# Optimization experiments

Hardware: AMD Instinct MI355X
Metric: run time of the kernel (lower is better)

The kernel has to match this reference:

```python
import jax, jax.numpy as jnp
import numpy as np

EMBED_DIM = 512
N_HEADS = 8
HEAD_DIM = EMBED_DIM // N_HEADS
B, S = 4, 2048

def gelu(x):
    # torch F.gelu default = exact erf gelu
    return jax.nn.gelu(x, approximate=False)

def setup_inputs() -> dict:
    key = jax.random.key(0)
    ks = jax.random.split(key, 9)
    sc = 1.0 / np.sqrt(EMBED_DIM)
    inp = {
        'x':   jax.random.normal(ks[0], (B, S, EMBED_DIM), dtype=jnp.float32),
        'Wq':  jax.random.uniform(ks[1], (EMBED_DIM, EMBED_DIM), jnp.float32, -sc, sc),
        'bq':  jax.random.uniform(ks[2], (EMBED_DIM,), jnp.float32, -sc, sc),
        'Wk':  jax.random.uniform(ks[3], (EMBED_DIM, EMBED_DIM), jnp.float32, -sc, sc),
        'bk':  jax.random.uniform(ks[4], (EMBED_DIM,), jnp.float32, -sc, sc),
        'Wv':  jax.random.uniform(ks[5], (EMBED_DIM, EMBED_DIM), jnp.float32, -sc, sc),
        'bv':  jax.random.uniform(ks[6], (EMBED_DIM,), jnp.float32, -sc, sc),
        'Wo':  jax.random.uniform(ks[7], (EMBED_DIM, EMBED_DIM), jnp.float32, -sc, sc),
        'bo':  jax.random.uniform(ks[8], (EMBED_DIM,), jnp.float32, -sc, sc),
    }
    return inp

def reference(x, Wq, bq, Wk, bk, Wv, bv, Wo, bo):
    Bsz, Ssz, _ = x.shape
    def proj(W, b):
        # [B,S,E] -> [B,H,S,D], GELU applied before head split (same math either way)
        h = gelu(jnp.einsum('bse,ef->bsf', x, W.T) + b)
        return h.reshape(Bsz, Ssz, N_HEADS, HEAD_DIM).transpose(0, 2, 1, 3)
    q = proj(Wq, bq)
    k = proj(Wk, bk)
    v = proj(Wv, bv)
    attn = jnp.einsum('bhid,bhjd->bhij', q, k) / np.sqrt(HEAD_DIM).astype(np.float32)
    attn = jax.nn.softmax(attn, axis=-1)
    o = jnp.einsum('bhij,bhjd->bhid', attn, v)
    o = o.transpose(0, 2, 1, 3).reshape(Bsz, Ssz, EMBED_DIM)
    return gelu(jnp.einsum('bse,ef->bsf', o, Wo.T) + bo)
```

## Files before the change

### kernel.cpp

```cpp
#include <hip/hip_runtime.h>
#include <hip/hip_bf16.h>

typedef __bf16 bf16_t;
typedef __bf16 bf16x4 __attribute__((ext_vector_type(4)));
typedef __bf16 bf16x8 __attribute__((ext_vector_type(8)));
typedef float  f32x4  __attribute__((ext_vector_type(4)));
typedef float  f32x8  __attribute__((ext_vector_type(8)));

#define EMBED 512
#define NH    8
#define HD    64
#define SEQ   2048
#define MTOT  8192
#define SCQ   0.18033688011112042f

__device__ __forceinline__ float gelu_f(float x) {
    return 0.5f * x * (1.0f + erff(x * 0.7071067811865475f));
}

__device__ __forceinline__ f32x4 mfma16(bf16x8 a, bf16x8 b, f32x4 c) {
    return __builtin_amdgcn_mfma_f32_16x16x32_bf16(a, b, c, 0, 0, 0);
}

__global__ __launch_bounds__(256)
void convert_kernel(const float* __restrict__ x,  const float* __restrict__ Wq,
                    const float* __restrict__ Wk, const float* __restrict__ Wv,
                    bf16_t* __restrict__ xb, bf16_t* __restrict__ wb)
{
    const int y = blockIdx.y;
    const float* src; bf16_t* dst;
    if (y < 16)      { src = x + (size_t)y * 262144; dst = xb + (size_t)y * 262144; }
    else if (y == 16){ src = Wq; dst = wb; }
    else if (y == 17){ src = Wk; dst = wb + 262144; }
    else             { src = Wv; dst = wb + 524288; }
    const int base = (blockIdx.x * 256 + threadIdx.x) * 16;
    const f32x8 a = *(const f32x8*)(src + base);
    const f32x8 b = *(const f32x8*)(src + base + 8);
    *(bf16x8*)(dst + base)     = __builtin_convertvector(a, bf16x8);
    *(bf16x8*)(dst + base + 8) = __builtin_convertvector(b, bf16x8);
}

template<int MODE, int NTILE>
__global__ __launch_bounds__(256, 3)
void gemm_gelu_kernel(const bf16_t* __restrict__ Xb,
                      const bf16_t* __restrict__ Wb,
                      const float*  __restrict__ Wf,
                      const float*  __restrict__ B0,
                      const float*  __restrict__ B1,
                      bf16_t* __restrict__ O0, bf16_t* __restrict__ O1,
                      bf16_t* __restrict__ O2, float* __restrict__ Of)
{
    constexpr int NTN = NTILE / 32;
    __shared__ __align__(16) bf16_t SMEM[128 * 72 + NTILE * 72];
    bf16_t* As = SMEM;
    bf16_t* Bs = SMEM + 128 * 72;
    const int tid  = threadIdx.x;
    const int lane = tid & 63, w = tid >> 6, quad = lane >> 4, l15 = lane & 15;
    const int m0 = blockIdx.x * 128;
    int mat, n0;
    if (MODE == 0) { mat = blockIdx.y >> 2; n0 = (blockIdx.y & 3) * 128; }
    else           { mat = 2;               n0 = blockIdx.y * NTILE; }
    const bf16_t* W  = (MODE == 2) ? nullptr
                                   : (Wb + (size_t)((MODE == 0) ? mat : 2) * 262144);
    const float*  Bi = (MODE == 0) ? (mat == 0 ? B0 : B1) : B0;

    const int wr = (w >> 1) * 64;
    const int wc = (w & 1) * (NTILE / 2);
    const int srow = tid >> 3, scol = (tid & 7) * 8;

    f32x4 acc[4][NTN];
#pragma unroll
    for (int a = 0; a < 4; ++a)
#pragma unroll
        for (int b = 0; b < NTN; ++b) acc[a][b] = f32x4{0.f, 0.f, 0.f, 0.f};

    bf16x8 xp[4];
    bf16x8 wpb[NTN];
    f32x8  wpf[NTN];

#pragma unroll
    for (int it = 0; it < 4; ++it)
        xp[it] = *(const bf16x8*)(Xb + (size_t)(m0 + it * 32 + srow) * EMBED + scol);
#pragma unroll
    for (int it = 0; it < NTN; ++it) {
        const int r = it * 32 + srow;
        if (MODE != 2) wpb[it] = *(const bf16x8*)(W + (size_t)(n0 + r) * EMBED + scol);
        else           wpf[it] = *(const f32x8*)(Wf + (size_t)(n0 + r) * EMBED + scol);
    }

#pragma unroll 1
    for (int kt = 0; kt < 8; ++kt) {
        __syncthreads();
#pragma unroll
        for (int it = 0; it < 4; ++it)
            *(bf16x8*)(As + (it * 32 + srow) * 72 + scol) = xp[it];
#pragma unroll
        for (int it = 0; it < NTN; ++it) {
            const int r = it * 32 + srow;
            if (MODE != 2) *(bf16x8*)(Bs + r * 72 + scol) = wpb[it];
            else *(bf16x8*)(Bs + r * 72 + scol) = __builtin_convertvector(wpf[it], bf16x8);
        }
        if (kt < 7) {
            const int k1 = (kt + 1) * 64;
#pragma unroll
            for (int it = 0; it < 4; ++it)
                xp[it] = *(const bf16x8*)(Xb + (size_t)(m0 + it * 32 + srow) * EMBED + k1 + scol);
#pragma unroll
            for (int it = 0; it < NTN; ++it) {
                const int r = it * 32 + srow;
                if (MODE != 2) wpb[it] = *(const bf16x8*)(W + (size_t)(n0 + r) * EMBED + k1 + scol);
                else           wpf[it] = *(const f32x8*)(Wf + (size_t)(n0 + r) * EMBED + k1 + scol);
            }
        }
        __syncthreads();
#pragma unroll
        for (int ks = 0; ks < 2; ++ks) {
            const int ko = (ks * 4 + quad) * 8;
            bf16x8 av[4], bv[NTN];
#pragma unroll
            for (int mt = 0; mt < 4; ++mt)
                av[mt] = *(const bf16x8*)(As + (wr + mt * 16 + l15) * 72 + ko);
#pragma unroll
            for (int nt = 0; nt < NTN; ++nt)
                bv[nt] = *(const bf16x8*)(Bs + (wc + nt * 16 + l15) * 72 + ko);
            if (MODE == 0) {
#pragma unroll
                for (int a = 0; a < NTN; ++a)
#pragma unroll
                    for (int b = 0; b < 4; ++b)
                        acc[a][b] = mfma16(bv[a], av[b], acc[a][b]);
            } else {
#pragma unroll
                for (int a = 0; a < 4; ++a)
#pragma unroll
                    for (int b = 0; b < NTN; ++b)
                        acc[a][b] = mfma16(av[a], bv[b], acc[a][b]);
            }
        }
    }

    if (MODE == 0) {
        bf16_t* T = SMEM;
        __syncthreads();
        const float scl = (mat == 0) ? SCQ : 1.0f;
#pragma unroll
        for (int at = 0; at < 4; ++at) {
            const int nb = wc + at * 16 + quad * 4;
            const f32x4 b4 = *(const f32x4*)(Bi + n0 + nb);
#pragma unroll
            for (int bt = 0; bt < 4; ++bt) {
                const int m = wr + bt * 16 + l15;
                bf16x4 pk;
#pragma unroll
                for (int i = 0; i < 4; ++i)
                    pk[i] = (bf16_t)(gelu_f(acc[at][bt][i] + b4[i]) * scl);
                *(bf16x4*)(T + m * 136 + nb) = pk;
            }
        }
        __syncthreads();
        bf16_t* O = (mat == 0) ? O0 : O1;
#pragma unroll
        for (int it = 0; it < 8; ++it) {
            const int chunk = w * 8 + it;
            const int hh = chunk >> 4, sg = chunk & 15;
            const int sr = lane >> 3, dc = (lane & 7) * 8;
            const int m = m0 + sg * 8 + sr;
            const int bb = m >> 11, s = m & (SEQ - 1);
            const int h = (n0 + hh * 64) >> 6;
            const bf16x8 v = *(const bf16x8*)(T + (sg * 8 + sr) * 136 + hh * 64 + dc);
            *(bf16x8*)(O + (((size_t)(bb * NH + h)) * SEQ + s) * HD + dc) = v;
        }
    } else if (MODE == 1) {
        bf16_t* T = SMEM;
        __syncthreads();
#pragma unroll
        for (int mt = 0; mt < 4; ++mt) {
            const int mloc = wr + mt * 16 + quad * 4;
#pragma unroll
            for (int nt = 0; nt < 4; ++nt) {
                const int nloc = wc + nt * 16 + l15;
                const float bs = Bi[n0 + nloc];
                bf16x4 pk;
#pragma unroll
                for (int i = 0; i < 4; ++i)
                    pk[i] = (bf16_t)gelu_f(acc[mt][nt][i] + bs);
                *(bf16x4*)(T + nloc * 136 + mloc) = pk;
            }
        }
        __syncthreads();
        const int bb = m0 >> 11, sbase = m0 & (SEQ - 1);
#pragma unroll
        for (int it = 0; it < 8; ++it) {
            const int chunk = w * 8 + it;
            const int r = lane >> 4, sc = (lane & 15) * 8;
            const int nloc = chunk * 4 + r;
            const int fc = n0 + nloc, h = fc >> 6, d = fc & 63;
            const bf16x8 v = *(const bf16x8*)(T + nloc * 136 + sc);
            *(bf16x8*)(O2 + ((size_t)(bb * NH + h) * HD + d) * SEQ + sbase + sc) = v;
        }
    } else {
#pragma unroll
        for (int mt = 0; mt < 4; ++mt) {
            const int mb = m0 + wr + mt * 16 + quad * 4;
#pragma unroll
            for (int nt = 0; nt < NTN; ++nt) {
                const int fc = n0 + wc + nt * 16 + l15;
                const float bs = Bi[fc];
#pragma unroll
                for (int i = 0; i < 4; ++i)
                    Of[(size_t)(mb + i) * EMBED + fc] = gelu_f(acc[mt][nt][i] + bs);
            }
        }
    }
}

__global__ __launch_bounds__(256, 2)
void flash_attn_kernel(const bf16_t* __restrict__ Q,
                       const bf16_t* __restrict__ K,
                       const bf16_t* __restrict__ Vt,
                       bf16_t* __restrict__ Og)
{
    __shared__ __align__(16) bf16_t Ks[2][64 * 72];
    __shared__ __align__(16) bf16_t Vs[2][64 * 72];
    __shared__ __align__(16) bf16_t Ps[4][32 * 72];

    const int tid  = threadIdx.x;
    const int lane = tid & 63, w = tid >> 6, quad = lane >> 4, l15 = lane & 15;
    const int bh = blockIdx.y;
    const int q0 = blockIdx.x * 128;
    const size_t baseQK = (size_t)bh * SEQ * HD;
    const size_t baseV  = (size_t)bh * HD * SEQ;
    const int wm = w * 32;

    bf16x8 qf[2][2];
#pragma unroll
    for (int mt = 0; mt < 2; ++mt)
#pragma unroll
        for (int ks = 0; ks < 2; ++ks)
            qf[mt][ks] = *(const bf16x8*)(Q + baseQK +
                (size_t)(q0 + wm + mt * 16 + l15) * HD + ks * 32 + quad * 8);

    float lsum[2] = {0.f, 0.f};
    f32x4 oacc[2][4];
#pragma unroll
    for (int mt = 0; mt < 2; ++mt)
#pragma unroll
        for (int nt = 0; nt < 4; ++nt) oacc[mt][nt] = f32x4{0.f, 0.f, 0.f, 0.f};

    bf16_t* Pw = Ps[w];
    const int r0 = tid >> 3, c0 = (tid & 7) * 8;
    bf16x8 kr0, kr1, vr0, vr1;

    kr0 = *(const bf16x8*)(K + baseQK + (size_t)r0 * HD + c0);
    kr1 = *(const bf16x8*)(K + baseQK + (size_t)(r0 + 32) * HD + c0);
    vr0 = *(const bf16x8*)(Vt + baseV + (size_t)r0 * SEQ + c0);
    vr1 = *(const bf16x8*)(Vt + baseV + (size_t)(r0 + 32) * SEQ + c0);
    *(bf16x8*)(Ks[0] + r0 * 72 + c0)        = kr0;
    *(bf16x8*)(Ks[0] + (r0 + 32) * 72 + c0) = kr1;
    *(bf16x8*)(Vs[0] + r0 * 72 + c0)        = vr0;
    *(bf16x8*)(Vs[0] + (r0 + 32) * 72 + c0) = vr1;
    kr0 = *(const bf16x8*)(K + baseQK + (size_t)(64 + r0) * HD + c0);
    kr1 = *(const bf16x8*)(K + baseQK + (size_t)(64 + r0 + 32) * HD + c0);
    vr0 = *(const bf16x8*)(Vt + baseV + (size_t)r0 * SEQ + 64 + c0);
    vr1 = *(const bf16x8*)(Vt + baseV + (size_t)(r0 + 32) * SEQ + 64 + c0);

#pragma unroll 1
    for (int t = 0; t < 32; ++t) {
        __syncthreads();
        if (t + 1 < 32) {
            bf16_t* Kn = Ks[(t + 1) & 1];
            bf16_t* Vn = Vs[(t + 1) & 1];
            *(bf16x8*)(Kn + r0 * 72 + c0)        = kr0;
            *(bf16x8*)(Kn + (r0 + 32) * 72 + c0) = kr1;
            *(bf16x8*)(Vn + r0 * 72 + c0)        = vr0;
            *(bf16x8*)(Vn + (r0 + 32) * 72 + c0) = vr1;
        }
        if (t + 2 < 32) {
            const int kv = (t + 2) * 64;
            kr0 = *(const bf16x8*)(K + baseQK + (size_t)(kv + r0) * HD + c0);
            kr1 = *(const bf16x8*)(K + baseQK + (size_t)(kv + r0 + 32) * HD + c0);
            vr0 = *(const bf16x8*)(Vt + baseV + (size_t)r0 * SEQ + kv + c0);
            vr1 = *(const bf16x8*)(Vt + baseV + (size_t)(r0 + 32) * SEQ + kv + c0);
        }

        const bf16_t* Kb = Ks[t & 1];
        const bf16_t* Vb = Vs[t & 1];

        f32x4 sf[2][4];
#pragma unroll
        for (int mt = 0; mt < 2; ++mt)
#pragma unroll
            for (int jt = 0; jt < 4; ++jt) sf[mt][jt] = f32x4{0.f, 0.f, 0.f, 0.f};
#pragma unroll
        for (int ks = 0; ks < 2; ++ks) {
            const int ko = ks * 32 + quad * 8;
#pragma unroll
            for (int jt = 0; jt < 4; ++jt) {
                const bf16x8 a = *(const bf16x8*)(Kb + (jt * 16 + l15) * 72 + ko);
                sf[0][jt] = mfma16(a, qf[0][ks], sf[0][jt]);
                sf[1][jt] = mfma16(a, qf[1][ks], sf[1][jt]);
            }
        }

#pragma unroll
        for (int mt = 0; mt < 2; ++mt)
#pragma unroll
            for (int jt = 0; jt < 4; ++jt) {
                f32x4 p;
#pragma unroll
                for (int i = 0; i < 4; ++i) {
                    p[i] = exp2f(sf[mt][jt][i] - 8.f);
                    lsum[mt] += p[i];
                }
                const bf16x4 pk = __builtin_convertvector(p, bf16x4);
                *(bf16x4*)(Pw + (mt * 16 + l15) * 72 + jt * 16 + quad * 4) = pk;
            }

#pragma unroll
        for (int c = 0; c < 2; ++c) {
            const int ko = c * 32 + quad * 8;
            const bf16x8 a0 = *(const bf16x8*)(Pw + l15 * 72 + ko);
            const bf16x8 a1 = *(const bf16x8*)(Pw + (16 + l15) * 72 + ko);
#pragma unroll
            for (int nt = 0; nt < 4; ++nt) {
                const bf16x8 b = *(const bf16x8*)(Vb + (nt * 16 + l15) * 72 + ko);
                oacc[0][nt] = mfma16(a0, b, oacc[0][nt]);
                oacc[1][nt] = mfma16(a1, b, oacc[1][nt]);
            }
        }
    }

    const int bidx = bh >> 3, h = bh & 7;
#pragma unroll
    for (int mt = 0; mt < 2; ++mt) {
        float rs = lsum[mt];
        rs += __shfl_xor(rs, 16);
        rs += __shfl_xor(rs, 32);
        float lf[4];
#pragma unroll
        for (int i = 0; i < 4; ++i)
            lf[i] = __shfl(rs, (lane & 48) | (quad * 4 + i));
#pragma unroll
        for (int nt = 0; nt < 4; ++nt)
#pragma unroll
            for (int i = 0; i < 4; ++i) {
                const int s = q0 + wm + mt * 16 + quad * 4 + i;
                const int d = nt * 16 + l15;
                Og[((size_t)(bidx * SEQ + s)) * EMBED + h * HD + d] =
                    (bf16_t)(oacc[mt][nt][i] / lf[i]);
            }
    }
}

extern "C" void kernel_launch(void* const* d_in, const int* in_sizes, int n_in,
                              void* d_out, int out_size, void* d_ws, size_t ws_size,
                              hipStream_t stream)
{
    const float* x  = (const float*)d_in[0];
    const float* Wq = (const float*)d_in[1];
    const float* bq = (const float*)d_in[2];
    const float* Wk = (const float*)d_in[3];
    const float* bk = (const float*)d_in[4];
    const float* Wv = (const float*)d_in[5];
    const float* bv = (const float*)d_in[6];
    const float* Wo = (const float*)d_in[7];
    const float* bo = (const float*)d_in[8];
    float* out = (float*)d_out;

    const size_t NE = (size_t)MTOT * EMBED;
    bf16_t* xb  = (bf16_t*)d_out;
    bf16_t* Qw  = (bf16_t*)d_out + NE;
    bf16_t* Kw  = (bf16_t*)d_ws;
    bf16_t* Vtw = Kw + NE;
    bf16_t* Ow  = Vtw + NE;
    bf16_t* Wb  = Ow;

    convert_kernel<<<dim3(64, 19), 256, 0, stream>>>(x, Wq, Wk, Wv, xb, Wb);
    gemm_gelu_kernel<0, 128><<<dim3(64, 8), 256, 0, stream>>>(
        xb, Wb, nullptr, bq, bk, Qw, Kw, nullptr, nullptr);
    gemm_gelu_kernel<1, 128><<<dim3(64, 4), 256, 0, stream>>>(
        xb, Wb, nullptr, bv, nullptr, nullptr, nullptr, Vtw, nullptr);
    flash_attn_kernel<<<dim3(16, 32), 256, 0, stream>>>(Qw, Kw, Vtw, Ow);
    gemm_gelu_kernel<2, 64><<<dim3(64, 8), 256, 0, stream>>>(
        Ow, nullptr, Wo, bo, nullptr, nullptr, nullptr, nullptr, out);
}
```

Measured before the change: 199.3 us.

## Fuse V projection into QK GEMM launch and unpad flash-attn K/V LDS

```diff
diff --git a/kernel.cpp b/kernel.cpp
--- a/kernel.cpp
+++ b/kernel.cpp
@@ -47,6 +47,7 @@
                       const float*  __restrict__ Wf,
                       const float*  __restrict__ B0,
                       const float*  __restrict__ B1,
+                      const float*  __restrict__ B2,
                       bf16_t* __restrict__ O0, bf16_t* __restrict__ O1,
                       bf16_t* __restrict__ O2, float* __restrict__ Of)
 {
@@ -59,10 +60,9 @@
     const int m0 = blockIdx.x * 128;
     int mat, n0;
     if (MODE == 0) { mat = blockIdx.y >> 2; n0 = (blockIdx.y & 3) * 128; }
-    else           { mat = 2;               n0 = blockIdx.y * NTILE; }
-    const bf16_t* W  = (MODE == 2) ? nullptr
-                                   : (Wb + (size_t)((MODE == 0) ? mat : 2) * 262144);
-    const float*  Bi = (MODE == 0) ? (mat == 0 ? B0 : B1) : B0;
+    else           { mat = 0;               n0 = blockIdx.y * NTILE; }
+    const bf16_t* W  = (MODE == 0) ? (Wb + (size_t)mat * 262144) : nullptr;
+    const float*  Bi = (MODE == 0) ? (mat == 0 ? B0 : (mat == 1 ? B1 : B2)) : B0;
 
     const int wr = (w >> 1) * 64;
     const int wc = (w & 1) * (NTILE / 2);
@@ -84,7 +84,7 @@
 #pragma unroll
     for (int it = 0; it < NTN; ++it) {
         const int r = it * 32 + srow;
-        if (MODE != 2) wpb[it] = *(const bf16x8*)(W + (size_t)(n0 + r) * EMBED + scol);
+        if (MODE == 0) wpb[it] = *(const bf16x8*)(W + (size_t)(n0 + r) * EMBED + scol);
         else           wpf[it] = *(const f32x8*)(Wf + (size_t)(n0 + r) * EMBED + scol);
     }
 
@@ -97,7 +97,7 @@
 #pragma unroll
         for (int it = 0; it < NTN; ++it) {
             const int r = it * 32 + srow;
-            if (MODE != 2) *(bf16x8*)(Bs + r * 72 + scol) = wpb[it];
+            if (MODE == 0) *(bf16x8*)(Bs + r * 72 + scol) = wpb[it];
             else *(bf16x8*)(Bs + r * 72 + scol) = __builtin_convertvector(wpf[it], bf16x8);
         }
         if (kt < 7) {
@@ -108,7 +108,7 @@
 #pragma unroll
             for (int it = 0; it < NTN; ++it) {
                 const int r = it * 32 + srow;
-                if (MODE != 2) wpb[it] = *(const bf16x8*)(W + (size_t)(n0 + r) * EMBED + k1 + scol);
+                if (MODE == 0) wpb[it] = *(const bf16x8*)(W + (size_t)(n0 + r) * EMBED + k1 + scol);
                 else           wpf[it] = *(const f32x8*)(Wf + (size_t)(n0 + r) * EMBED + k1 + scol);
             }
         }
@@ -142,61 +142,61 @@
     if (MODE == 0) {
         bf16_t* T = SMEM;
         __syncthreads();
-        const float scl = (mat == 0) ? SCQ : 1.0f;
-#pragma unroll
-        for (int at = 0; at < 4; ++at) {
-            const int nb = wc + at * 16 + quad * 4;
-            const f32x4 b4 = *(const f32x4*)(Bi + n0 + nb);
-#pragma unroll
-            for (int bt = 0; bt < 4; ++bt) {
-                const int m = wr + bt * 16 + l15;
-                bf16x4 pk;
-#pragma unroll
-                for (int i = 0; i < 4; ++i)
-                    pk[i] = (bf16_t)(gelu_f(acc[at][bt][i] + b4[i]) * scl);
-                *(bf16x4*)(T + m * 136 + nb) = pk;
-            }
-        }
-        __syncthreads();
-        bf16_t* O = (mat == 0) ? O0 : O1;
-#pragma unroll
-        for (int it = 0; it < 8; ++it) {
-            const int chunk = w * 8 + it;
-            const int hh = chunk >> 4, sg = chunk & 15;
-            const int sr = lane >> 3, dc = (lane & 7) * 8;
-            const int m = m0 + sg * 8 + sr;
-            const int bb = m >> 11, s = m & (SEQ - 1);
-            const int h = (n0 + hh * 64) >> 6;
-            const bf16x8 v = *(const bf16x8*)(T + (sg * 8 + sr) * 136 + hh * 64 + dc);
-            *(bf16x8*)(O + (((size_t)(bb * NH + h)) * SEQ + s) * HD + dc) = v;
-        }
-    } else if (MODE == 1) {
-        bf16_t* T = SMEM;
-        __syncthreads();
-#pragma unroll
-        for (int mt = 0; mt < 4; ++mt) {
-            const int mloc = wr + mt * 16 + quad * 4;
-#pragma unroll
-            for (int nt = 0; nt < 4; ++nt) {
-                const int nloc = wc + nt * 16 + l15;
-                const float bs = Bi[n0 + nloc];
-                bf16x4 pk;
-#pragma unroll
-                for (int i = 0; i < 4; ++i)
-                    pk[i] = (bf16_t)gelu_f(acc[mt][nt][i] + bs);
-                *(bf16x4*)(T + nloc * 136 + mloc) = pk;
-            }
-        }
-        __syncthreads();
-        const int bb = m0 >> 11, sbase = m0 & (SEQ - 1);
-#pragma unroll
-        for (int it = 0; it < 8; ++it) {
-            const int chunk = w * 8 + it;
-            const int r = lane >> 4, sc = (lane & 15) * 8;
-            const int nloc = chunk * 4 + r;
-            const int fc = n0 + nloc, h = fc >> 6, d = fc & 63;
-            const bf16x8 v = *(const bf16x8*)(T + nloc * 136 + sc);
-            *(bf16x8*)(O2 + ((size_t)(bb * NH + h) * HD + d) * SEQ + sbase + sc) = v;
+        if (mat < 2) {
+            const float scl = (mat == 0) ? SCQ : 1.0f;
+#pragma unroll
+            for (int at = 0; at < 4; ++at) {
+                const int nb = wc + at * 16 + quad * 4;
+                const f32x4 b4 = *(const f32x4*)(Bi + n0 + nb);
+#pragma unroll
+                for (int bt = 0; bt < 4; ++bt) {
+                    const int m = wr + bt * 16 + l15;
+                    bf16x4 pk;
+#pragma unroll
+                    for (int i = 0; i < 4; ++i)
+                        pk[i] = (bf16_t)(gelu_f(acc[at][bt][i] + b4[i]) * scl);
+                    *(bf16x4*)(T + m * 136 + nb) = pk;
+                }
+            }
+        } else {
+#pragma unroll
+            for (int at = 0; at < 4; ++at) {
+                const int nb = wc + at * 16 + quad * 4;
+                const f32x4 b4 = *(const f32x4*)(Bi + n0 + nb);
+#pragma unroll
+                for (int bt = 0; bt < 4; ++bt) {
+                    const int m = wr + bt * 16 + l15;
+#pragma unroll
+                    for (int i = 0; i < 4; ++i)
+                        T[(nb + i) * 136 + m] = (bf16_t)gelu_f(acc[at][bt][i] + b4[i]);
+                }
+            }
+        }
+        __syncthreads();
+        if (mat < 2) {
+            bf16_t* O = (mat == 0) ? O0 : O1;
+#pragma unroll
+            for (int it = 0; it < 8; ++it) {
+                const int chunk = w * 8 + it;
+                const int hh = chunk >> 4, sg = chunk & 15;
+                const int sr = lane >> 3, dc = (lane & 7) * 8;
+                const int m = m0 + sg * 8 + sr;
+                const int bb = m >> 11, s = m & (SEQ - 1);
+                const int h = (n0 + hh * 64) >> 6;
+                const bf16x8 v = *(const bf16x8*)(T + (sg * 8 + sr) * 136 + hh * 64 + dc);
+                *(bf16x8*)(O + (((size_t)(bb * NH + h)) * SEQ + s) * HD + dc) = v;
+            }
+        } else {
+            const int bb = m0 >> 11, sbase = m0 & (SEQ - 1);
+#pragma unroll
+            for (int it = 0; it < 8; ++it) {
+                const int chunk = w * 8 + it;
+                const int r = lane >> 4, sc = (lane & 15) * 8;
+                const int nloc = chunk * 4 + r;
+                const int fc = n0 + nloc, h = fc >> 6, d = fc & 63;
+                const bf16x8 v = *(const bf16x8*)(T + nloc * 136 + sc);
+                *(bf16x8*)(O2 + ((size_t)(bb * NH + h) * HD + d) * SEQ + sbase + sc) = v;
+            }
         }
     } else {
 #pragma unroll
@@ -214,14 +214,14 @@
     }
 }
 
-__global__ __launch_bounds__(256, 2)
+__global__ __launch_bounds__(256, 3)
 void flash_attn_kernel(const bf16_t* __restrict__ Q,
                        const bf16_t* __restrict__ K,
                        const bf16_t* __restrict__ Vt,
                        bf16_t* __restrict__ Og)
 {
-    __shared__ __align__(16) bf16_t Ks[2][64 * 72];
-    __shared__ __align__(16) bf16_t Vs[2][64 * 72];
+    __shared__ __align__(16) bf16_t Ks[2][64 * 64];
+    __shared__ __align__(16) bf16_t Vs[2][64 * 64];
     __shared__ __align__(16) bf16_t Ps[4][32 * 72];
 
     const int tid  = threadIdx.x;
@@ -255,10 +255,10 @@
     kr1 = *(const bf16x8*)(K + baseQK + (size_t)(r0 + 32) * HD + c0);
     vr0 = *(const bf16x8*)(Vt + baseV + (size_t)r0 * SEQ + c0);
     vr1 = *(const bf16x8*)(Vt + baseV + (size_t)(r0 + 32) * SEQ + c0);
-    *(bf16x8*)(Ks[0] + r0 * 72 + c0)        = kr0;
-    *(bf16x8*)(Ks[0] + (r0 + 32) * 72 + c0) = kr1;
-    *(bf16x8*)(Vs[0] + r0 * 72 + c0)        = vr0;
-    *(bf16x8*)(Vs[0] + (r0 + 32) * 72 + c0) = vr1;
+    *(bf16x8*)(Ks[0] + r0 * 64 + c0)        = kr0;
+    *(bf16x8*)(Ks[0] + (r0 + 32) * 64 + c0) = kr1;
+    *(bf16x8*)(Vs[0] + r0 * 64 + c0)        = vr0;
+    *(bf16x8*)(Vs[0] + (r0 + 32) * 64 + c0) = vr1;
     kr0 = *(const bf16x8*)(K + baseQK + (size_t)(64 + r0) * HD + c0);
     kr1 = *(const bf16x8*)(K + baseQK + (size_t)(64 + r0 + 32) * HD + c0);
     vr0 = *(const bf16x8*)(Vt + baseV + (size_t)r0 * SEQ + 64 + c0);
@@ -270,10 +270,10 @@
         if (t + 1 < 32) {
             bf16_t* Kn = Ks[(t + 1) & 1];
             bf16_t* Vn = Vs[(t + 1) & 1];
-            *(bf16x8*)(Kn + r0 * 72 + c0)        = kr0;
-            *(bf16x8*)(Kn + (r0 + 32) * 72 + c0) = kr1;
-            *(bf16x8*)(Vn + r0 * 72 + c0)        = vr0;
-            *(bf16x8*)(Vn + (r0 + 32) * 72 + c0) = vr1;
+            *(bf16x8*)(Kn + r0 * 64 + c0)        = kr0;
+            *(bf16x8*)(Kn + (r0 + 32) * 64 + c0) = kr1;
+            *(bf16x8*)(Vn + r0 * 64 + c0)        = vr0;
+            *(bf16x8*)(Vn + (r0 + 32) * 64 + c0) = vr1;
         }
         if (t + 2 < 32) {
             const int kv = (t + 2) * 64;
@@ -296,7 +296,7 @@
             const int ko = ks * 32 + quad * 8;
 #pragma unroll
             for (int jt = 0; jt < 4; ++jt) {
-                const bf16x8 a = *(const bf16x8*)(Kb + (jt * 16 + l15) * 72 + ko);
+                const bf16x8 a = *(const bf16x8*)(Kb + (jt * 16 + l15) * 64 + ko);
                 sf[0][jt] = mfma16(a, qf[0][ks], sf[0][jt]);
                 sf[1][jt] = mfma16(a, qf[1][ks], sf[1][jt]);
             }
@@ -323,7 +323,7 @@
             const bf16x8 a1 = *(const bf16x8*)(Pw + (16 + l15) * 72 + ko);
 #pragma unroll
             for (int nt = 0; nt < 4; ++nt) {
-                const bf16x8 b = *(const bf16x8*)(Vb + (nt * 16 + l15) * 72 + ko);
+                const bf16x8 b = *(const bf16x8*)(Vb + (nt * 16 + l15) * 64 + ko);
                 oacc[0][nt] = mfma16(a0, b, oacc[0][nt]);
                 oacc[1][nt] = mfma16(a1, b, oacc[1][nt]);
             }
@@ -376,11 +376,9 @@
     bf16_t* Wb  = Ow;
 
     convert_kernel<<<dim3(64, 19), 256, 0, stream>>>(x, Wq, Wk, Wv, xb, Wb);
-    gemm_gelu_kernel<0, 128><<<dim3(64, 8), 256, 0, stream>>>(
-        xb, Wb, nullptr, bq, bk, Qw, Kw, nullptr, nullptr);
-    gemm_gelu_kernel<1, 128><<<dim3(64, 4), 256, 0, stream>>>(
-        xb, Wb, nullptr, bv, nullptr, nullptr, nullptr, Vtw, nullptr);
+    gemm_gelu_kernel<0, 128><<<dim3(64, 12), 256, 0, stream>>>(
+        xb, Wb, nullptr, bq, bk, bv, Qw, Kw, Vtw, nullptr);
     flash_attn_kernel<<<dim3(16, 32), 256, 0, stream>>>(Qw, Kw, Vtw, Ow);
     gemm_gelu_kernel<2, 64><<<dim3(64, 8), 256, 0, stream>>>(
-        Ow, nullptr, Wo, bo, nullptr, nullptr, nullptr, nullptr, out);
-}
+        Ow, nullptr, Wo, bo, nullptr, nullptr, nullptr, nullptr, nullptr, out);
+}
```

After: 197.5 us. No clear change (-0.9%).
